# Performance work log

Hardware: AMD Instinct MI355X
Metric: run time of the kernel (lower is better)

The kernel has to match this reference:

```python
import jax, jax.numpy as jnp
import numpy as np

B, S, D = 2, 2048, 1024
N_HEADS = 16
PAT_HEADS = N_HEADS // 4          # MultiheadAttention num_heads = 4
HEAD_DIM = D // PAT_HEADS         # 256
SPARSITY_RATIO = 0.1
MEMORY_PRESSURE = 0.5
NEG_INF = -1e9


def setup_inputs() -> dict:
    key = jax.random.key(0)
    ks = jax.random.split(key, 16)
    sd = 1.0 / np.sqrt(D)
    sh = 1.0 / np.sqrt(D // 4)
    inp = {
        "q": jax.random.normal(ks[0], (B, S, D), jnp.float32),
        "k": jax.random.normal(ks[1], (B, S, D), jnp.float32),
        "v": jax.random.normal(ks[2], (B, S, D), jnp.float32),
        # sparsity predictor: Linear(D, D//4) -> ReLU -> Linear(D//4, 1) -> Sigmoid
        "w1": jax.random.uniform(ks[3], (D, D // 4), jnp.float32, -sd, sd),
        "b1": jax.random.uniform(ks[4], (D // 4,), jnp.float32, -sd, sd),
        "w2": jax.random.uniform(ks[5], (D // 4, 1), jnp.float32, -sh, sh),
        "b2": jax.random.uniform(ks[6], (1,), jnp.float32, -sh, sh),
        # MultiheadAttention in_proj (split) + out_proj, stored [in, out]
        "wq": jax.random.uniform(ks[7], (D, D), jnp.float32, -sd, sd),
        "bq": jnp.zeros((D,), jnp.float32),
        "wk": jax.random.uniform(ks[8], (D, D), jnp.float32, -sd, sd),
        "bk": jnp.zeros((D,), jnp.float32),
        "wv": jax.random.uniform(ks[9], (D, D), jnp.float32, -sd, sd),
        "bv": jnp.zeros((D,), jnp.float32),
        "wo": jax.random.uniform(ks[10], (D, D), jnp.float32, -sd, sd),
        "bo": jnp.zeros((D,), jnp.float32),
    }
    return inp


def reference(q, k, v, w1, b1, w2, b2, wq, bq, wk, bk, wv, bv, wo, bo):
    # learned importance scores -> boolean mask of active tokens
    h = jax.nn.relu(q @ w1 + b1)                       # [B,S,D//4]
    scores = jax.nn.sigmoid(h @ w2 + b2)[..., 0]       # [B,S]
    threshold = SPARSITY_RATIO * (1.0 + MEMORY_PRESSURE)
    mask = scores > threshold                          # [B,S] bool

    # original module flattens all active tokens across batch into ONE
    # sequence and runs MHA over that subset; we express the identical math
    # with a fixed-shape masked attention over the flattened [B*S] tokens.
    N = B * S
    mf = mask.reshape(N)                               # [N]
    qf = q.reshape(N, D)
    kf = k.reshape(N, D)
    vf = v.reshape(N, D)

    qp = (qf @ wq + bq).reshape(N, PAT_HEADS, HEAD_DIM)
    kp = (kf @ wk + bk).reshape(N, PAT_HEADS, HEAD_DIM)
    vp = (vf @ wv + bv).reshape(N, PAT_HEADS, HEAD_DIM)

    scale = 1.0 / np.sqrt(HEAD_DIM)
    logits = jnp.einsum("nhd,mhd->hnm", qp * scale, kp)   # [H,N,N]
    logits = jnp.where(mf[None, None, :], logits, NEG_INF)  # only active keys
    attn = jax.nn.softmax(logits, axis=-1)
    ctx = jnp.einsum("hnm,mhd->nhd", attn, vp).reshape(N, D)
    out = ctx @ wo + bo                                 # [N,D]

    # scatter back: inactive query positions stay zero
    out = jnp.where(mf[:, None], out, 0.0)
    return out.reshape(B, S, D)
```

## Files before the change

### kernel.cpp

```cpp
#include <hip/hip_runtime.h>
#include <hip/hip_bf16.h>
#include <math.h>

typedef __bf16 bf16x8 __attribute__((ext_vector_type(8)));
typedef __bf16 bf16x4 __attribute__((ext_vector_type(4)));
typedef float  f32x4  __attribute__((ext_vector_type(4)));
typedef short  s16x8  __attribute__((ext_vector_type(8)));

#define N_TOK  4096
#define DMODEL 1024
#define NHEAD  4
#define DHEAD  256

__device__ __forceinline__ f32x4 mfma16x16(bf16x8 a, bf16x8 b, f32x4 c) {
    return __builtin_amdgcn_mfma_f32_16x16x32_bf16(a, b, c, 0, 0, 0);
}

__device__ __forceinline__ void gload_lds16(const void* gsrc, void* ldst) {
    __builtin_amdgcn_global_load_lds(
        (const __attribute__((address_space(1))) void*)gsrc,
        (__attribute__((address_space(3))) void*)ldst, 16, 0, 0);
}

struct CvtArgs { const float* src[3]; __bf16* dst[3]; };
__global__ __launch_bounds__(256)
void cvt_bf16_kernel(CvtArgs a)
{
    const float* in = a.src[blockIdx.y];
    __bf16* out = a.dst[blockIdx.y];
    size_t i8 = ((size_t)blockIdx.x * 256 + threadIdx.x) * 8;
    f32x4 t0 = *(const f32x4*)(in + i8);
    f32x4 t1 = *(const f32x4*)(in + i8 + 4);
    bf16x8 b;
    #pragma unroll
    for (int j = 0; j < 4; ++j) { b[j] = (__bf16)t0[j]; b[j + 4] = (__bf16)t1[j]; }
    *(bf16x8*)(out + i8) = b;
}

__device__ __forceinline__ void transposew_body(const float* __restrict__ in,
                                                __bf16* __restrict__ out, int C)
{
    __shared__ __align__(16) __bf16 tile[64 * 72];
    const int tid = threadIdx.x;
    const int r0 = blockIdx.x * 64;
    const int c0 = blockIdx.y * 64;
    if (c0 >= C) return;
    #pragma unroll
    for (int it = 0; it < 4; ++it) {
        int i = tid + it * 256;
        int row = i >> 4, c4 = i & 15;
        f32x4 v = *(const f32x4*)(in + (size_t)(r0 + row) * C + c0 + c4 * 4);
        #pragma unroll
        for (int j = 0; j < 4; ++j)
            tile[(c4 * 4 + j) * 72 + row] = (__bf16)v[j];
    }
    __syncthreads();
    #pragma unroll
    for (int it = 0; it < 2; ++it) {
        int i = tid + it * 256;
        int col = i >> 3, ch = i & 7;
        s16x8 v = *(const s16x8*)(&tile[col * 72 + ch * 8]);
        *(s16x8*)((short*)out + (size_t)(c0 + col) * 1024 + r0 + ch * 8) = v;
    }
}

__global__ __launch_bounds__(256)
void transposew_kernel(const float* __restrict__ in, __bf16* __restrict__ out, int C)
{
    transposew_body(in, out, C);
}

struct TWArgs { const float* src[4]; __bf16* dst[4]; int C[4]; };
__global__ __launch_bounds__(256)
void transposew_batch_kernel(TWArgs a)
{
    int z = blockIdx.z;
    transposew_body(a.src[z], a.dst[z], a.C[z]);
}

struct GemmDesc {
    const __bf16* A; const __bf16* B; const float* bias; __bf16* C;
    int lda, ldb, ldc, gx, nblocks, relu, biasrow; float scale;
};
struct FusedArgs { GemmDesc d[4]; };

__global__ __launch_bounds__(256, 2)
void gemm_fused(FusedArgs fa)
{
    __shared__ __align__(16) short As[2][128 * 64];
    __shared__ __align__(16) short Bs[2][128 * 64];

    int b = blockIdx.x, z = 0;
    while (b >= fa.d[z].nblocks) { b -= fa.d[z].nblocks; ++z; }
    const GemmDesc D = fa.d[z];
    const int m0 = (b % D.gx) * 128;
    const int n0 = (b / D.gx) * 128;

    const int tid  = threadIdx.x;
    const int lane = tid & 63;
    const int wv   = tid >> 6;
    const int c16  = lane & 15;
    const int quad = lane >> 4;
    const int swz  = c16 & 7;
    const int wr   = wv >> 1;
    const int wc   = wv & 1;

    f32x4 acc[4][4];
    #pragma unroll
    for (int i = 0; i < 4; ++i)
        #pragma unroll
        for (int j = 0; j < 4; ++j)
            acc[i][j] = (f32x4){0.f, 0.f, 0.f, 0.f};

    const int sRow = lane >> 3;
    const int sCh  = (lane & 7) ^ (sRow & 7);

    auto issue = [&](short* Abuf, short* Bbuf, int k0) {
        #pragma unroll
        for (int g = 0; g < 4; ++g) {
            int row = 32 * wv + 8 * g + sRow;
            const char* src = (const char*)(D.A + (size_t)(m0 + row) * D.lda + k0) + sCh * 16;
            gload_lds16(src, (char*)Abuf + (32 * wv + 8 * g) * 128);
        }
        #pragma unroll
        for (int g = 0; g < 4; ++g) {
            int row = 32 * wv + 8 * g + sRow;
            const char* src = (const char*)(D.B + (size_t)(n0 + row) * D.ldb + k0) + sCh * 16;
            gload_lds16(src, (char*)Bbuf + (32 * wv + 8 * g) * 128);
        }
    };
    auto compute = [&](const short* Abuf, const short* Bbuf) {
        __builtin_amdgcn_s_setprio(1);
        #pragma unroll
        for (int ks = 0; ks < 2; ++ks) {
            bf16x8 af[4], bfr[4];
            int slot = ((ks * 4 + quad) ^ swz) * 16;
            #pragma unroll
            for (int t = 0; t < 4; ++t)
                af[t] = *(const bf16x8*)((const char*)Abuf + (wr * 64 + t * 16 + c16) * 128 + slot);
            #pragma unroll
            for (int t = 0; t < 4; ++t)
                bfr[t] = *(const bf16x8*)((const char*)Bbuf + (wc * 64 + t * 16 + c16) * 128 + slot);
            #pragma unroll
            for (int tm = 0; tm < 4; ++tm)
                #pragma unroll
                for (int tn = 0; tn < 4; ++tn)
                    acc[tm][tn] = mfma16x16(af[tm], bfr[tn], acc[tm][tn]);
        }
        __builtin_amdgcn_s_setprio(0);
    };

    issue(As[0], Bs[0], 0);
    __syncthreads();

    #pragma unroll 1
    for (int t = 0; t < 16; t += 2) {
        if (t + 1 < 16) issue(As[1], Bs[1], (t + 1) << 6);
        compute(As[0], Bs[0]);
        __syncthreads();
        if (t + 2 < 16) issue(As[0], Bs[0], (t + 2) << 6);
        compute(As[1], Bs[1]);
        __syncthreads();
    }

    #pragma unroll
    for (int tm = 0; tm < 4; ++tm) {
        #pragma unroll
        for (int rr = 0; rr < 4; ++rr) {
            int row = m0 + wr * 64 + tm * 16 + quad * 4 + rr;
            float rbv = D.biasrow ? D.bias[row] : 0.0f;
            #pragma unroll
            for (int tn = 0; tn < 4; ++tn) {
                int col = n0 + wc * 64 + tn * 16 + c16;
                float bb = D.biasrow ? rbv : D.bias[col];
                float val = (acc[tm][tn][rr] + bb) * D.scale;
                if (D.relu) val = fmaxf(val, 0.0f);
                D.C[(size_t)row * D.ldc + col] = (__bf16)val;
            }
        }
    }
}

template<typename OutT, bool BIASROW>
__global__ __launch_bounds__(256, 2)
void gemm_bt(const __bf16* __restrict__ A, int lda,
             const __bf16* __restrict__ B, int ldb,
             const float* __restrict__ bias,
             OutT* __restrict__ C, int ldc,
             float scale, int relu, const float* __restrict__ rowmask, int K)
{
    __shared__ __align__(16) short As[2][128 * 64];
    __shared__ __align__(16) short Bs[2][128 * 64];
    const int tid  = threadIdx.x;
    const int lane = tid & 63;
    const int wv   = tid >> 6;
    const int c16  = lane & 15;
    const int quad = lane >> 4;
    const int swz  = c16 & 7;
    const int wr   = wv >> 1;
    const int wc   = wv & 1;
    const int m0 = blockIdx.x * 128;
    const int n0 = blockIdx.y * 128;

    f32x4 acc[4][4];
    #pragma unroll
    for (int i = 0; i < 4; ++i)
        #pragma unroll
        for (int j = 0; j < 4; ++j)
            acc[i][j] = (f32x4){0.f, 0.f, 0.f, 0.f};

    const int sRow = lane >> 3;
    const int sCh  = (lane & 7) ^ (sRow & 7);

    auto issue = [&](short* Abuf, short* Bbuf, int k0) {
        #pragma unroll
        for (int g = 0; g < 4; ++g) {
            int row = 32 * wv + 8 * g + sRow;
            const char* src = (const char*)(A + (size_t)(m0 + row) * lda + k0) + sCh * 16;
            gload_lds16(src, (char*)Abuf + (32 * wv + 8 * g) * 128);
        }
        #pragma unroll
        for (int g = 0; g < 4; ++g) {
            int row = 32 * wv + 8 * g + sRow;
            const char* src = (const char*)(B + (size_t)(n0 + row) * ldb + k0) + sCh * 16;
            gload_lds16(src, (char*)Bbuf + (32 * wv + 8 * g) * 128);
        }
    };
    auto compute = [&](const short* Abuf, const short* Bbuf) {
        __builtin_amdgcn_s_setprio(1);
        #pragma unroll
        for (int ks = 0; ks < 2; ++ks) {
            bf16x8 af[4], bfr[4];
            int slot = ((ks * 4 + quad) ^ swz) * 16;
            #pragma unroll
            for (int t = 0; t < 4; ++t)
                af[t] = *(const bf16x8*)((const char*)Abuf + (wr * 64 + t * 16 + c16) * 128 + slot);
            #pragma unroll
            for (int t = 0; t < 4; ++t)
                bfr[t] = *(const bf16x8*)((const char*)Bbuf + (wc * 64 + t * 16 + c16) * 128 + slot);
            #pragma unroll
            for (int tm = 0; tm < 4; ++tm)
                #pragma unroll
                for (int tn = 0; tn < 4; ++tn)
                    acc[tm][tn] = mfma16x16(af[tm], bfr[tn], acc[tm][tn]);
        }
        __builtin_amdgcn_s_setprio(0);
    };

    const int nt = K >> 6;
    issue(As[0], Bs[0], 0);
    __syncthreads();

    #pragma unroll 1
    for (int t = 0; t < nt; t += 2) {
        if (t + 1 < nt) issue(As[1], Bs[1], (t + 1) << 6);
        compute(As[0], Bs[0]);
        __syncthreads();
        if (t + 1 < nt) {
            if (t + 2 < nt) issue(As[0], Bs[0], (t + 2) << 6);
            compute(As[1], Bs[1]);
            __syncthreads();
        }
    }

    #pragma unroll
    for (int tm = 0; tm < 4; ++tm) {
        #pragma unroll
        for (int rr = 0; rr < 4; ++rr) {
            int row = m0 + wr * 64 + tm * 16 + quad * 4 + rr;
            float mk = rowmask ? rowmask[row] : 1.0f;
            float rbv = BIASROW ? bias[row] : 0.0f;
            #pragma unroll
            for (int tn = 0; tn < 4; ++tn) {
                int col = n0 + wc * 64 + tn * 16 + c16;
                float b = BIASROW ? rbv : bias[col];
                float val = (acc[tm][tn][rr] + b) * scale;
                if (relu) val = fmaxf(val, 0.0f);
                val *= mk;
                C[(size_t)row * ldc + col] = (OutT)val;
            }
        }
    }
}

__global__ void score_mask_kernel(const __bf16* __restrict__ h,
                                  const float* __restrict__ w2,
                                  const float* __restrict__ b2,
                                  float* __restrict__ maskf)
{
    int lane = threadIdx.x & 63;
    int tok  = blockIdx.x * 4 + (threadIdx.x >> 6);
    const __bf16* hr = h + (size_t)tok * 256;
    float s = 0.f;
    #pragma unroll
    for (int j = 0; j < 4; ++j) {
        int c = j * 64 + lane;
        s += (float)hr[c] * w2[c];
    }
    #pragma unroll
    for (int o = 1; o < 64; o <<= 1) s += __shfl_xor(s, o);
    if (lane == 0) {
        float x = s + b2[0];
        maskf[tok] = (x > -1.7346010553881064f) ? 1.0f : 0.0f;
    }
}

__global__ __launch_bounds__(512, 1)
void attn_kernel(const __bf16* __restrict__ qp, const __bf16* __restrict__ kp,
                 const __bf16* __restrict__ vpT, const float* __restrict__ maskf,
                 __bf16* __restrict__ O0, __bf16* __restrict__ O1,
                 float* __restrict__ lbuf)
{
    __shared__ __align__(16) short Ks[2][64 * 256];
    __shared__ __align__(16) short Vs[2][256 * 64];
    __shared__ __align__(16) short PsA[8 * 16 * 64];

    const int tid  = threadIdx.x;
    const int lane = tid & 63;
    const int wv   = tid >> 6;
    const int c16  = lane & 15;
    const int quad = lane >> 4;
    const int swz  = c16 & 7;

    const int d    = blockIdx.x;
    const int orig = ((d & 7) << 5) | (d >> 3);
    const int qb   = orig & 31;
    const int head = (orig >> 5) & 3;
    const int ksp  = orig >> 7;
    const int kbase = ksp * 2048;
    const int kend  = kbase + 2048;
    const int q0   = qb * 128 + wv * 16;
    short* Ps = PsA + wv * 16 * 64;
    __bf16* Ob = ksp ? O1 : O0;

    bf16x8 qf[8];
    #pragma unroll
    for (int c = 0; c < 8; ++c)
        qf[c] = *(const bf16x8*)(qp + (size_t)(q0 + c16) * DMODEL + head * DHEAD + c * 32 + quad * 8);

    f32x4 o[16];
    #pragma unroll
    for (int t = 0; t < 16; ++t) o[t] = (f32x4){0.f, 0.f, 0.f, 0.f};
    float psum[4] = {0.f, 0.f, 0.f, 0.f};

    const int kRow0 = wv * 8 + (lane >> 5);
    const int kCh   = lane & 31;
    const int vRow0 = wv * 32 + (lane >> 3);
    const int vCh   = (lane & 7) ^ ((lane >> 3) & 7);

    auto issue = [&](int buf, int n0) {
        #pragma unroll
        for (int g = 0; g < 4; ++g) {
            int key = kRow0 + g * 2;
            int c   = kCh ^ (key & 7);
            const char* src = (const char*)(kp + (size_t)(n0 + key) * DMODEL + head * DHEAD) + c * 16;
            gload_lds16(src, (char*)Ks[buf] + (wv * 8 + g * 2) * 512);
        }
        #pragma unroll
        for (int g = 0; g < 4; ++g) {
            int row = vRow0 + g * 8;
            const char* src = (const char*)(vpT + (size_t)(head * DHEAD + row) * N_TOK + n0) + vCh * 16;
            gload_lds16(src, (char*)Vs[buf] + (wv * 32 + g * 8) * 128);
        }
    };

    issue(0, kbase);
    __syncthreads();
    int cur = 0;

    #pragma unroll 1
    for (int n0 = kbase; n0 < kend; n0 += 64) {
        if (n0 + 64 < kend) issue(cur ^ 1, n0 + 64);
        const short* Kb = Ks[cur];
        const short* Vb = Vs[cur];

        f32x4 s[4];
        #pragma unroll
        for (int kt = 0; kt < 4; ++kt) s[kt] = (f32x4){0.f, 0.f, 0.f, 0.f};
        __builtin_amdgcn_s_setprio(1);
        #pragma unroll
        for (int c = 0; c < 8; ++c)
            #pragma unroll
            for (int kt = 0; kt < 4; ++kt) {
                bf16x8 bfr = *(const bf16x8*)(&Kb[(kt * 16 + c16) * 256 + (((c * 4 + quad) ^ swz) << 3)]);
                s[kt] = mfma16x16(qf[c], bfr, s[kt]);
            }
        __builtin_amdgcn_s_setprio(0);

        #pragma unroll
        for (int kt = 0; kt < 4; ++kt) {
            float biasv = (maskf[n0 + kt * 16 + c16] - 1.0f) * 1e9f;
            #pragma unroll
            for (int r = 0; r < 4; ++r) {
                float p = __expf(s[kt][r] + biasv);
                psum[r] += p;
                int qrow = quad * 4 + r;
                int ch = (kt * 2 + (c16 >> 3)) ^ (qrow & 7);
                *(__bf16*)&Ps[qrow * 64 + ch * 8 + swz] = (__bf16)p;
            }
        }

        __builtin_amdgcn_s_waitcnt(0xc07f);

        __builtin_amdgcn_s_setprio(1);
        #pragma unroll
        for (int kstep = 0; kstep < 2; ++kstep) {
            bf16x8 pf = *(const bf16x8*)(&Ps[c16 * 64 + (((kstep * 4 + quad) ^ swz) << 3)]);
            #pragma unroll
            for (int t = 0; t < 16; ++t) {
                bf16x8 vf = *(const bf16x8*)(&Vb[(t * 16 + c16) * 64 + (((kstep * 4 + quad) ^ swz) << 3)]);
                o[t] = mfma16x16(pf, vf, o[t]);
            }
        }
        __builtin_amdgcn_s_setprio(0);
        __syncthreads();
        cur ^= 1;
    }

    float inv[4];
    #pragma unroll
    for (int r = 0; r < 4; ++r) {
        float t = psum[r];
        t += __shfl_xor(t, 1);
        t += __shfl_xor(t, 2);
        t += __shfl_xor(t, 4);
        t += __shfl_xor(t, 8);
        if (c16 == 0)
            lbuf[(size_t)(ksp * NHEAD + head) * N_TOK + q0 + quad * 4 + r] = t;
        inv[r] = 1.0f / t;
    }
    #pragma unroll
    for (int t = 0; t < 16; ++t)
        #pragma unroll
        for (int r = 0; r < 4; ++r) {
            float val = o[t][r] * inv[r];
            Ob[(size_t)(q0 + quad * 4 + r) * DMODEL + head * DHEAD + t * 16 + c16] = (__bf16)val;
        }
}

__global__ void combine_kernel(const __bf16* __restrict__ O0,
                               const __bf16* __restrict__ O1,
                               const float* __restrict__ lbuf,
                               __bf16* __restrict__ out)
{
    int idx  = blockIdx.x * 256 + threadIdx.x;
    int tok  = idx >> 7;
    int g    = idx & 127;
    int head = g >> 5;
    float a = lbuf[(size_t)head * N_TOK + tok];
    float b = lbuf[(size_t)(NHEAD + head) * N_TOK + tok];
    float w0 = a / (a + b);
    float w1 = 1.0f - w0;
    size_t off = (size_t)tok * DMODEL + g * 8;
    bf16x8 x = *(const bf16x8*)(O0 + off);
    bf16x8 y = *(const bf16x8*)(O1 + off);
    bf16x8 z;
    #pragma unroll
    for (int j = 0; j < 8; ++j) z[j] = (__bf16)(w0 * (float)x[j] + w1 * (float)y[j]);
    *(bf16x8*)(out + off) = z;
}

extern "C" void kernel_launch(void* const* d_in, const int* in_sizes, int n_in,
                              void* d_out, int out_size, void* d_ws, size_t ws_size,
                              hipStream_t stream)
{
    (void)in_sizes; (void)n_in; (void)out_size;
    const float* q  = (const float*)d_in[0];
    const float* k  = (const float*)d_in[1];
    const float* v  = (const float*)d_in[2];
    const float* w1 = (const float*)d_in[3];
    const float* b1 = (const float*)d_in[4];
    const float* w2 = (const float*)d_in[5];
    const float* b2 = (const float*)d_in[6];
    const float* wq = (const float*)d_in[7];
    const float* bq = (const float*)d_in[8];
    const float* wk = (const float*)d_in[9];
    const float* bk = (const float*)d_in[10];
    const float* wvw = (const float*)d_in[11];
    const float* bv = (const float*)d_in[12];
    const float* wo = (const float*)d_in[13];
    const float* bo = (const float*)d_in[14];

    if (ws_size < 35667968u + 8388608u + 131072u) return;

    char* ws = (char*)d_ws;
    float*  maskf = (float*)ws;
    __bf16* hbuf  = (__bf16*)(ws + 16384);
    __bf16* qp    = (__bf16*)(ws + 16384 + 2097152);
    __bf16* kpb   = qp  + 4194304;
    __bf16* vpT   = kpb + 4194304;
    __bf16* ctx   = vpT + 4194304;
    __bf16* O1    = (__bf16*)(ws + 35667968u);
    float*  lbuf  = (float*)(ws + 35667968u + 8388608u);

    __bf16* wqT = (__bf16*)d_out;
    __bf16* wkT = wqT + 1048576;
    __bf16* wvT = wkT + 1048576;
    __bf16* w1T = wvT + 1048576;
    __bf16* vbf = (__bf16*)((char*)d_out + 6815744u);
    __bf16* woT = hbuf;
    __bf16* qbf = O1;
    __bf16* kbf = ctx;

    CvtArgs ca;
    ca.src[0] = q;  ca.dst[0] = qbf;
    ca.src[1] = k;  ca.dst[1] = kbf;
    ca.src[2] = v;  ca.dst[2] = vbf;
    cvt_bf16_kernel<<<dim3(2048, 3), 256, 0, stream>>>(ca);

    TWArgs ta;
    ta.src[0] = w1;  ta.dst[0] = w1T;  ta.C[0] = 256;
    ta.src[1] = wq;  ta.dst[1] = wqT;  ta.C[1] = 1024;
    ta.src[2] = wk;  ta.dst[2] = wkT;  ta.C[2] = 1024;
    ta.src[3] = wvw; ta.dst[3] = wvT;  ta.C[3] = 1024;
    transposew_batch_kernel<<<dim3(16, 16, 4), 256, 0, stream>>>(ta);

    FusedArgs fa;
    fa.d[0] = { qbf, w1T, b1, hbuf, 1024, 1024,  256, 32,  64, 1, 0, 1.0f };
    fa.d[1] = { qbf, wqT, bq, qp,   1024, 1024, 1024, 32, 256, 0, 0, 0.0625f };
    fa.d[2] = { kbf, wkT, bk, kpb,  1024, 1024, 1024, 32, 256, 0, 0, 1.0f };
    fa.d[3] = { wvT, vbf, bv, vpT,  1024, 1024, 4096,  8, 256, 0, 1, 1.0f };
    gemm_fused<<<dim3(832), 256, 0, stream>>>(fa);

    score_mask_kernel<<<1024, 256, 0, stream>>>(hbuf, w2, b2, maskf);
    transposew_kernel<<<dim3(16, 16), 256, 0, stream>>>(wo, woT, 1024);

    attn_kernel<<<dim3(256), 512, 0, stream>>>(qp, kpb, vpT, maskf, ctx, O1, lbuf);
    combine_kernel<<<2048, 256, 0, stream>>>(ctx, O1, lbuf, ctx);

    gemm_bt<float, false><<<dim3(32, 8), 256, 0, stream>>>(
        ctx, 1024, woT, 1024, bo, (float*)d_out, 1024, 1.0f, 0, maskf, 1024);
}
```

Measured before the change: 307.4 us.

## Process two query tiles per wave and split keys four ways in attention

Each wave now handles 32 query rows as two 16-row sub-tiles, so every K and V fragment read from LDS feeds two MFMAs instead of one. To keep 256 blocks with the larger per-wave tile, the key range is split into four 1024-key chunks, and the combine kernel merges four partial outputs using their row sums. K is now single-buffered and loaded after a barrier, while V stays double-buffered; the P scratch uses padded rows instead of an XOR swizzle. Workspace buffers are reassigned to hold the extra partials, and the wo transpose is moved after combine. The doubled accumulators raise register pressure, and the single K buffer adds a synchronization point.

```diff
diff --git a/kernel.cpp b/kernel.cpp
--- a/kernel.cpp
+++ b/kernel.cpp
@@ -309,11 +309,12 @@
 void attn_kernel(const __bf16* __restrict__ qp, const __bf16* __restrict__ kp,
                  const __bf16* __restrict__ vpT, const float* __restrict__ maskf,
                  __bf16* __restrict__ O0, __bf16* __restrict__ O1,
+                 __bf16* __restrict__ O2, __bf16* __restrict__ O3,
                  float* __restrict__ lbuf)
 {
-    __shared__ __align__(16) short Ks[2][64 * 256];
+    __shared__ __align__(16) short Ks[64 * 256];
     __shared__ __align__(16) short Vs[2][256 * 64];
-    __shared__ __align__(16) short PsA[8 * 16 * 64];
+    __shared__ __align__(16) short PsA[8 * 32 * 72];
 
     const int tid  = threadIdx.x;
     const int lane = tid & 63;
@@ -323,123 +324,144 @@
     const int swz  = c16 & 7;
 
     const int d    = blockIdx.x;
-    const int orig = ((d & 7) << 5) | (d >> 3);
-    const int qb   = orig & 31;
-    const int head = (orig >> 5) & 3;
-    const int ksp  = orig >> 7;
-    const int kbase = ksp * 2048;
-    const int kend  = kbase + 2048;
-    const int q0   = qb * 128 + wv * 16;
-    short* Ps = PsA + wv * 16 * 64;
-    __bf16* Ob = ksp ? O1 : O0;
-
-    bf16x8 qf[8];
-    #pragma unroll
-    for (int c = 0; c < 8; ++c)
-        qf[c] = *(const bf16x8*)(qp + (size_t)(q0 + c16) * DMODEL + head * DHEAD + c * 32 + quad * 8);
-
-    f32x4 o[16];
-    #pragma unroll
-    for (int t = 0; t < 16; ++t) o[t] = (f32x4){0.f, 0.f, 0.f, 0.f};
-    float psum[4] = {0.f, 0.f, 0.f, 0.f};
+    const int g    = d & 7;
+    const int tt   = d >> 3;
+    const int head = g >> 1;
+    const int ksp  = (g & 1) * 2 + (tt >> 4);
+    const int qb   = tt & 15;
+    const int kbase = ksp * 1024;
+    const int q0w  = qb * 256 + wv * 32;
+    short* Ps = PsA + wv * 32 * 72;
+    __bf16* Ob = (ksp == 0) ? O0 : (ksp == 1) ? O1 : (ksp == 2) ? O2 : O3;
+
+    bf16x8 qf[2][8];
+    #pragma unroll
+    for (int sub = 0; sub < 2; ++sub)
+        #pragma unroll
+        for (int c = 0; c < 8; ++c)
+            qf[sub][c] = *(const bf16x8*)(qp + (size_t)(q0w + sub * 16 + c16) * DMODEL + head * DHEAD + c * 32 + quad * 8);
+
+    f32x4 o[2][16];
+    #pragma unroll
+    for (int sub = 0; sub < 2; ++sub)
+        #pragma unroll
+        for (int t = 0; t < 16; ++t) o[sub][t] = (f32x4){0.f, 0.f, 0.f, 0.f};
+    float psum[2][4] = {{0.f, 0.f, 0.f, 0.f}, {0.f, 0.f, 0.f, 0.f}};
 
     const int kRow0 = wv * 8 + (lane >> 5);
     const int kCh   = lane & 31;
     const int vRow0 = wv * 32 + (lane >> 3);
     const int vCh   = (lane & 7) ^ ((lane >> 3) & 7);
 
-    auto issue = [&](int buf, int n0) {
-        #pragma unroll
-        for (int g = 0; g < 4; ++g) {
-            int key = kRow0 + g * 2;
+    auto issueK = [&](int n0) {
+        #pragma unroll
+        for (int gg = 0; gg < 4; ++gg) {
+            int key = kRow0 + gg * 2;
             int c   = kCh ^ (key & 7);
             const char* src = (const char*)(kp + (size_t)(n0 + key) * DMODEL + head * DHEAD) + c * 16;
-            gload_lds16(src, (char*)Ks[buf] + (wv * 8 + g * 2) * 512);
-        }
-        #pragma unroll
-        for (int g = 0; g < 4; ++g) {
-            int row = vRow0 + g * 8;
+            gload_lds16(src, (char*)Ks + (wv * 8 + gg * 2) * 512);
+        }
+    };
+    auto issueV = [&](int buf, int n0) {
+        #pragma unroll
+        for (int gg = 0; gg < 4; ++gg) {
+            int row = vRow0 + gg * 8;
             const char* src = (const char*)(vpT + (size_t)(head * DHEAD + row) * N_TOK + n0) + vCh * 16;
-            gload_lds16(src, (char*)Vs[buf] + (wv * 32 + g * 8) * 128);
+            gload_lds16(src, (char*)Vs[buf] + (wv * 32 + gg * 8) * 128);
         }
     };
 
-    issue(0, kbase);
+    issueK(kbase);
+    issueV(0, kbase);
     __syncthreads();
-    int cur = 0;
 
     #pragma unroll 1
-    for (int n0 = kbase; n0 < kend; n0 += 64) {
-        if (n0 + 64 < kend) issue(cur ^ 1, n0 + 64);
-        const short* Kb = Ks[cur];
-        const short* Vb = Vs[cur];
-
-        f32x4 s[4];
-        #pragma unroll
-        for (int kt = 0; kt < 4; ++kt) s[kt] = (f32x4){0.f, 0.f, 0.f, 0.f};
+    for (int it = 0; it < 16; ++it) {
+        const int n0  = kbase + it * 64;
+        const int buf = it & 1;
+        if (it + 1 < 16) issueV(buf ^ 1, n0 + 64);
+
+        #pragma unroll
+        for (int kh = 0; kh < 2; ++kh) {
+            f32x4 s0[2], s1[2];
+            #pragma unroll
+            for (int k2 = 0; k2 < 2; ++k2) {
+                s0[k2] = (f32x4){0.f, 0.f, 0.f, 0.f};
+                s1[k2] = (f32x4){0.f, 0.f, 0.f, 0.f};
+            }
+            __builtin_amdgcn_s_setprio(1);
+            #pragma unroll
+            for (int c = 0; c < 8; ++c)
+                #pragma unroll
+                for (int k2 = 0; k2 < 2; ++k2) {
+                    int kt = kh * 2 + k2;
+                    bf16x8 bfr = *(const bf16x8*)(&Ks[(kt * 16 + c16) * 256 + (((c * 4 + quad) ^ swz) << 3)]);
+                    s0[k2] = mfma16x16(qf[0][c], bfr, s0[k2]);
+                    s1[k2] = mfma16x16(qf[1][c], bfr, s1[k2]);
+                }
+            __builtin_amdgcn_s_setprio(0);
+            #pragma unroll
+            for (int k2 = 0; k2 < 2; ++k2) {
+                int kt = kh * 2 + k2;
+                float biasv = (maskf[n0 + kt * 16 + c16] - 1.0f) * 1e9f;
+                #pragma unroll
+                for (int r = 0; r < 4; ++r) {
+                    float p0 = __expf(s0[k2][r] + biasv);
+                    float p1 = __expf(s1[k2][r] + biasv);
+                    psum[0][r] += p0;
+                    psum[1][r] += p1;
+                    *(__bf16*)&Ps[(quad * 4 + r) * 72 + kt * 16 + c16] = (__bf16)p0;
+                    *(__bf16*)&Ps[(16 + quad * 4 + r) * 72 + kt * 16 + c16] = (__bf16)p1;
+                }
+            }
+        }
+        __syncthreads();
+
+        if (it + 1 < 16) issueK(n0 + 64);
         __builtin_amdgcn_s_setprio(1);
         #pragma unroll
-        for (int c = 0; c < 8; ++c)
-            #pragma unroll
-            for (int kt = 0; kt < 4; ++kt) {
-                bf16x8 bfr = *(const bf16x8*)(&Kb[(kt * 16 + c16) * 256 + (((c * 4 + quad) ^ swz) << 3)]);
-                s[kt] = mfma16x16(qf[c], bfr, s[kt]);
-            }
-        __builtin_amdgcn_s_setprio(0);
-
-        #pragma unroll
-        for (int kt = 0; kt < 4; ++kt) {
-            float biasv = (maskf[n0 + kt * 16 + c16] - 1.0f) * 1e9f;
-            #pragma unroll
-            for (int r = 0; r < 4; ++r) {
-                float p = __expf(s[kt][r] + biasv);
-                psum[r] += p;
-                int qrow = quad * 4 + r;
-                int ch = (kt * 2 + (c16 >> 3)) ^ (qrow & 7);
-                *(__bf16*)&Ps[qrow * 64 + ch * 8 + swz] = (__bf16)p;
-            }
-        }
-
-        __builtin_amdgcn_s_waitcnt(0xc07f);
-
-        __builtin_amdgcn_s_setprio(1);
-        #pragma unroll
         for (int kstep = 0; kstep < 2; ++kstep) {
-            bf16x8 pf = *(const bf16x8*)(&Ps[c16 * 64 + (((kstep * 4 + quad) ^ swz) << 3)]);
+            bf16x8 pf0 = *(const bf16x8*)(&Ps[c16 * 72 + kstep * 32 + quad * 8]);
+            bf16x8 pf1 = *(const bf16x8*)(&Ps[(16 + c16) * 72 + kstep * 32 + quad * 8]);
             #pragma unroll
             for (int t = 0; t < 16; ++t) {
-                bf16x8 vf = *(const bf16x8*)(&Vb[(t * 16 + c16) * 64 + (((kstep * 4 + quad) ^ swz) << 3)]);
-                o[t] = mfma16x16(pf, vf, o[t]);
+                bf16x8 vf = *(const bf16x8*)(&Vs[buf][(t * 16 + c16) * 64 + (((kstep * 4 + quad) ^ swz) << 3)]);
+                o[0][t] = mfma16x16(pf0, vf, o[0][t]);
+                o[1][t] = mfma16x16(pf1, vf, o[1][t]);
             }
         }
         __builtin_amdgcn_s_setprio(0);
         __syncthreads();
-        cur ^= 1;
-    }
-
-    float inv[4];
-    #pragma unroll
-    for (int r = 0; r < 4; ++r) {
-        float t = psum[r];
-        t += __shfl_xor(t, 1);
-        t += __shfl_xor(t, 2);
-        t += __shfl_xor(t, 4);
-        t += __shfl_xor(t, 8);
-        if (c16 == 0)
-            lbuf[(size_t)(ksp * NHEAD + head) * N_TOK + q0 + quad * 4 + r] = t;
-        inv[r] = 1.0f / t;
-    }
-    #pragma unroll
-    for (int t = 0; t < 16; ++t)
+    }
+
+    #pragma unroll
+    for (int sub = 0; sub < 2; ++sub) {
+        float inv[4];
         #pragma unroll
         for (int r = 0; r < 4; ++r) {
-            float val = o[t][r] * inv[r];
-            Ob[(size_t)(q0 + quad * 4 + r) * DMODEL + head * DHEAD + t * 16 + c16] = (__bf16)val;
-        }
+            float tsum = psum[sub][r];
+            tsum += __shfl_xor(tsum, 1);
+            tsum += __shfl_xor(tsum, 2);
+            tsum += __shfl_xor(tsum, 4);
+            tsum += __shfl_xor(tsum, 8);
+            if (c16 == 0)
+                lbuf[(size_t)(ksp * NHEAD + head) * N_TOK + q0w + sub * 16 + quad * 4 + r] = tsum;
+            inv[r] = 1.0f / tsum;
+        }
+        #pragma unroll
+        for (int t = 0; t < 16; ++t)
+            #pragma unroll
+            for (int r = 0; r < 4; ++r) {
+                float val = o[sub][t][r] * inv[r];
+                Ob[(size_t)(q0w + sub * 16 + quad * 4 + r) * DMODEL + head * DHEAD + t * 16 + c16] = (__bf16)val;
+            }
+    }
 }
 
 __global__ void combine_kernel(const __bf16* __restrict__ O0,
                                const __bf16* __restrict__ O1,
+                               const __bf16* __restrict__ O2,
+                               const __bf16* __restrict__ O3,
                                const float* __restrict__ lbuf,
                                __bf16* __restrict__ out)
 {
@@ -447,16 +469,20 @@
     int tok  = idx >> 7;
     int g    = idx & 127;
     int head = g >> 5;
-    float a = lbuf[(size_t)head * N_TOK + tok];
-    float b = lbuf[(size_t)(NHEAD + head) * N_TOK + tok];
-    float w0 = a / (a + b);
-    float w1 = 1.0f - w0;
+    float l0 = lbuf[(size_t)(0 * NHEAD + head) * N_TOK + tok];
+    float l1 = lbuf[(size_t)(1 * NHEAD + head) * N_TOK + tok];
+    float l2 = lbuf[(size_t)(2 * NHEAD + head) * N_TOK + tok];
+    float l3 = lbuf[(size_t)(3 * NHEAD + head) * N_TOK + tok];
+    float inv = 1.0f / (l0 + l1 + l2 + l3);
     size_t off = (size_t)tok * DMODEL + g * 8;
-    bf16x8 x = *(const bf16x8*)(O0 + off);
-    bf16x8 y = *(const bf16x8*)(O1 + off);
+    bf16x8 a = *(const bf16x8*)(O0 + off);
+    bf16x8 b = *(const bf16x8*)(O1 + off);
+    bf16x8 c = *(const bf16x8*)(O2 + off);
+    bf16x8 dd = *(const bf16x8*)(O3 + off);
     bf16x8 z;
     #pragma unroll
-    for (int j = 0; j < 8; ++j) z[j] = (__bf16)(w0 * (float)x[j] + w1 * (float)y[j]);
+    for (int j = 0; j < 8; ++j)
+        z[j] = (__bf16)((l0 * (float)a[j] + l1 * (float)b[j] + l2 * (float)c[j] + l3 * (float)dd[j]) * inv);
     *(bf16x8*)(out + off) = z;
 }
 
@@ -486,18 +512,20 @@
     char* ws = (char*)d_ws;
     float*  maskf = (float*)ws;
     __bf16* hbuf  = (__bf16*)(ws + 16384);
+    float*  lbuf  = (float*)(ws + 16384);
     __bf16* qp    = (__bf16*)(ws + 16384 + 2097152);
     __bf16* kpb   = qp  + 4194304;
     __bf16* vpT   = kpb + 4194304;
     __bf16* ctx   = vpT + 4194304;
     __bf16* O1    = (__bf16*)(ws + 35667968u);
-    float*  lbuf  = (float*)(ws + 35667968u + 8388608u);
 
     __bf16* wqT = (__bf16*)d_out;
     __bf16* wkT = wqT + 1048576;
     __bf16* wvT = wkT + 1048576;
     __bf16* w1T = wvT + 1048576;
     __bf16* vbf = (__bf16*)((char*)d_out + 6815744u);
+    __bf16* O2  = (__bf16*)d_out;
+    __bf16* O3  = (__bf16*)((char*)d_out + 8388608u);
     __bf16* woT = hbuf;
     __bf16* qbf = O1;
     __bf16* kbf = ctx;
@@ -523,11 +551,11 @@
     gemm_fused<<<dim3(832), 256, 0, stream>>>(fa);
 
     score_mask_kernel<<<1024, 256, 0, stream>>>(hbuf, w2, b2, maskf);
+
+    attn_kernel<<<dim3(256), 512, 0, stream>>>(qp, kpb, vpT, maskf, ctx, O1, O2, O3, lbuf);
+    combine_kernel<<<2048, 256, 0, stream>>>(ctx, O1, O2, O3, lbuf, ctx);
+
     transposew_kernel<<<dim3(16, 16), 256, 0, stream>>>(wo, woT, 1024);
-
-    attn_kernel<<<dim3(256), 512, 0, stream>>>(qp, kpb, vpT, maskf, ctx, O1, lbuf);
-    combine_kernel<<<2048, 256, 0, stream>>>(ctx, O1, lbuf, ctx);
-
     gemm_bt<float, false><<<dim3(32, 8), 256, 0, stream>>>(
         ctx, 1024, woT, 1024, bo, (float*)d_out, 1024, 1.0f, 0, maskf, 1024);
 }
```

After: 315.2 us. 2.5% more time.
